# Performance work log

Measured on AMD Instinct MI355X. Metric: run time of the kernel, lower is better.

Reference implementation:

```python
import jax, jax.numpy as jnp
import numpy as np

B, C_IN, H, W = 16, 1024, 32, 32
D_CODE, K = 1024, 2048  # codebook_dim, codebook_size


def setup_inputs() -> dict:
    key = jax.random.key(0)
    k1, k2, k3, k4 = jax.random.split(key, 4)
    x = jax.random.normal(k1, (B, C_IN, H, W), dtype=jnp.float32)
    # 1x1 conv kernel stored as (out=D_CODE, in=C_IN); scaled like torch conv init
    conv_w = jax.random.normal(k2, (D_CODE, C_IN), dtype=jnp.float32) / np.sqrt(C_IN)
    conv_b = jax.random.normal(k3, (D_CODE,), dtype=jnp.float32) * 0.01
    codebook = jax.random.normal(k4, (D_CODE, K), dtype=jnp.float32)
    return {"x": x, "conv_w": conv_w, "conv_b": conv_b, "codebook": codebook}


def reference(x, conv_w, conv_b, codebook):
    # 1x1 conv projection: (B, C_IN, H, W) -> (B, D_CODE, H, W)
    xp = jnp.einsum('bchw,dc->bdhw', x, conv_w) + conv_b[None, :, None, None]

    b, d, h, w = xp.shape
    # flatten spatial: (N, D) with N = B*H*W (matches 'b d h w -> (b h w) d')
    xf = jnp.transpose(xp, (0, 2, 3, 1)).reshape(-1, d)

    # pairwise squared distances to codebook columns: (N, K)
    dist = (jnp.sum(xf * xf, axis=1, keepdims=True)
            - 2.0 * (xf @ codebook)
            + jnp.sum(codebook * codebook, axis=0, keepdims=True))
    indices = jnp.argmin(dist, axis=1).reshape(b, h, w)  # (B, H, W)

    # gather codes: codebook.T is (K, D)
    quant_hw_d = codebook.T[indices]  # (B, H, W, D)
    quant = jnp.transpose(quant_hw_d, (0, 3, 1, 2))  # (B, D, H, W)

    # commitment loss (quantized detached)
    diff = jnp.mean((jax.lax.stop_gradient(quant) - xp) ** 2)

    # straight-through estimator
    quant_st = xp + jax.lax.stop_gradient(quant - xp)
    return quant_st, diff, indices
```

## Files before the change

### kernel.cpp

```cpp
#include <hip/hip_runtime.h>
#include <stdint.h>

#define BATCH 16
#define CIN   1024
#define HWSZ  1024
#define NPOS  16384
#define DCODE 1024
#define KCB   2048

#define OUT_QUANT 0
#define OUT_DIFF  16777216
#define OUT_IDX   16777217

#define OFF_PACKED 0u
#define OFF_CNORM  131072u
#define OFF_DIFF   139264u
#define OFF_WH     262144u
#define OFF_WL     2359296u
#define OFF_CBH    4456448u
#define OFF_CBL    8650752u
#define OFF_DYN    12845056u

typedef _Float16 f16x8 __attribute__((ext_vector_type(8)));
typedef float f32x4 __attribute__((ext_vector_type(4)));
typedef int i32x4 __attribute__((ext_vector_type(4)));
union H4 { _Float16 h[4]; uint2 u; };
union H8 { _Float16 h[8]; uint4 u; };
union QU { uint4 u; uint16_t v[8]; };
union B16 { char c[16]; uint4 u; };

__device__ __forceinline__ void gl_lds16(const void* g, void* l) {
  __builtin_amdgcn_global_load_lds(
      (const __attribute__((address_space(1))) uint32_t*)g,
      (__attribute__((address_space(3))) uint32_t*)l, 16, 0, 0);
}

__global__ void k_init(unsigned long long* __restrict__ packed, double* __restrict__ diffsum) {
  int i = blockIdx.x * 256 + threadIdx.x;
  if (i < NPOS) packed[i] = 0xFFFFFFFFFFFFFFFFull;
  if (i == 0) *diffsum = 0.0;
}

__global__ __launch_bounds__(256) void k_prep_w(const float* __restrict__ w,
                                                _Float16* __restrict__ wh, _Float16* __restrict__ wl) {
  const int d = blockIdx.x;
  const int c = threadIdx.x * 4;
  float4 v = *(const float4*)&w[(size_t)d * CIN + c];
  H4 hh, ll;
  float vv[4] = {v.x, v.y, v.z, v.w};
  #pragma unroll
  for (int i = 0; i < 4; ++i) {
    _Float16 h = (_Float16)vv[i];
    hh.h[i] = h;
    ll.h[i] = (_Float16)(vv[i] - (float)h);
  }
  *(uint2*)&wh[(size_t)d * CIN + c] = hh.u;
  *(uint2*)&wl[(size_t)d * CIN + c] = ll.u;
}

__global__ __launch_bounds__(256) void k_prep_cb(const float* __restrict__ cb,
                                                 _Float16* __restrict__ cbh, _Float16* __restrict__ cbl,
                                                 char* __restrict__ cq) {
  __shared__ float ts[64][65];
  const int t = threadIdx.x;
  const int k0 = blockIdx.x * 64, d0 = blockIdx.y * 64;
  #pragma unroll
  for (int i = 0; i < 4; ++i) {
    const int r = i * 16 + (t >> 4);
    float4 v = *(const float4*)&cb[(size_t)(d0 + r) * KCB + k0 + (t & 15) * 4];
    ts[r][(t & 15) * 4 + 0] = v.x; ts[r][(t & 15) * 4 + 1] = v.y;
    ts[r][(t & 15) * 4 + 2] = v.z; ts[r][(t & 15) * 4 + 3] = v.w;
  }
  __syncthreads();
  const int j = t >> 2;
  const int q = t & 3;
  H8 hh[2], ll[2];
  B16 qb;
  #pragma unroll
  for (int e = 0; e < 16; ++e) {
    float xv = ts[q * 16 + e][j];
    _Float16 h = (_Float16)xv;
    hh[e >> 3].h[e & 7] = h;
    ll[e >> 3].h[e & 7] = (_Float16)(xv - (float)h);
    int qi = (int)rintf(xv * 20.f);
    qi = qi > 127 ? 127 : (qi < -127 ? -127 : qi);
    qb.c[e] = (char)qi;
  }
  size_t o = (size_t)(k0 + j) * DCODE + d0 + q * 16;
  *(uint4*)&cbh[o] = hh[0].u; *(uint4*)&cbh[o + 8] = hh[1].u;
  *(uint4*)&cbl[o] = ll[0].u; *(uint4*)&cbl[o + 8] = ll[1].u;
  if (cq) *(uint4*)&cq[o] = qb.u;
}

__global__ __launch_bounds__(256) void k_prep_x(const float* __restrict__ x,
                                                _Float16* __restrict__ xh, _Float16* __restrict__ xl,
                                                int n_base) {
  __shared__ float ts[64][65];
  const int t = threadIdx.x;
  const int nt0 = blockIdx.x * 64;
  const int c0 = blockIdx.y * 64;
  const int ng = n_base + nt0;
  const int b = ng >> 10, hw0 = ng & 1023;
  #pragma unroll
  for (int i = 0; i < 4; ++i) {
    const int r = i * 16 + (t >> 4);
    float4 v = *(const float4*)&x[((size_t)b * CIN + c0 + r) * HWSZ + hw0 + (t & 15) * 4];
    ts[r][(t & 15) * 4 + 0] = v.x; ts[r][(t & 15) * 4 + 1] = v.y;
    ts[r][(t & 15) * 4 + 2] = v.z; ts[r][(t & 15) * 4 + 3] = v.w;
  }
  __syncthreads();
  const int j = t >> 2;
  const int q = t & 3;
  H8 hh[2], ll[2];
  #pragma unroll
  for (int e = 0; e < 16; ++e) {
    float xv = ts[q * 16 + e][j];
    _Float16 h = (_Float16)xv;
    hh[e >> 3].h[e & 7] = h;
    ll[e >> 3].h[e & 7] = (_Float16)(xv - (float)h);
  }
  size_t o = (size_t)(nt0 + j) * CIN + c0 + q * 16;
  *(uint4*)&xh[o] = hh[0].u; *(uint4*)&xh[o + 8] = hh[1].u;
  *(uint4*)&xl[o] = ll[0].u; *(uint4*)&xl[o + 8] = ll[1].u;
}

__global__ __launch_bounds__(256) void k_prep_xq(const _Float16* __restrict__ xph,
                                                 char* __restrict__ xq) {
  const size_t base = ((size_t)blockIdx.x * 256 + threadIdx.x) * 16;
  H8 a, b;
  a.u = *(const uint4*)&xph[base];
  b.u = *(const uint4*)&xph[base + 8];
  B16 qb;
  #pragma unroll
  for (int i = 0; i < 8; ++i) {
    int qi = (int)rintf((float)a.h[i] * 20.f);
    qi = qi > 127 ? 127 : (qi < -127 ? -127 : qi);
    qb.c[i] = (char)qi;
    int qj = (int)rintf((float)b.h[i] * 20.f);
    qj = qj > 127 ? 127 : (qj < -127 ? -127 : qj);
    qb.c[8 + i] = (char)qj;
  }
  *(uint4*)&xq[base] = qb.u;
}

__global__ __launch_bounds__(256) void k_cnorm2(const _Float16* __restrict__ cbh,
                                                const _Float16* __restrict__ cbl,
                                                float* __restrict__ cnorm) {
  __shared__ double rd[256];
  const int k = blockIdx.x;
  const int t = threadIdx.x;
  H4 hh, ll;
  hh.u = *(const uint2*)&cbh[(size_t)k * DCODE + t * 4];
  ll.u = *(const uint2*)&cbl[(size_t)k * DCODE + t * 4];
  double s = 0.0;
  #pragma unroll
  for (int i = 0; i < 4; ++i) {
    float v = (float)hh.h[i] + (float)ll.h[i];
    s += (double)v * v;
  }
  rd[t] = s;
  __syncthreads();
  for (int st = 128; st > 0; st >>= 1) {
    if (t < st) rd[t] += rd[t + st];
    __syncthreads();
  }
  if (t == 0) cnorm[k] = (float)rd[0];
}

template <int EPI, int NKTT>
__global__ __launch_bounds__(512, 2) void k_gemm_u(
    const _Float16* __restrict__ aH, const _Float16* __restrict__ aL,
    const _Float16* __restrict__ bH, const _Float16* __restrict__ bL,
    const float* __restrict__ bias,
    _Float16* __restrict__ oH, _Float16* __restrict__ oL,
    const float* __restrict__ cnorm, unsigned long long* __restrict__ packed,
    uint16_t* __restrict__ dqout, int n_base) {
  __shared__ __align__(16) _Float16 smem[65536];
  const int tid = threadIdx.x;
  const int lane = tid & 63, wid = tid >> 6;
  const int wm = wid >> 2, wn = wid & 3;
  const int m0 = blockIdx.x * 256;
  const int n0 = blockIdx.y * 256;
  const int kg = lane >> 4;
  const int l7 = lane & 7;

  const int srow = lane >> 3;
  const int sg = l7 ^ srow;
  size_t srcA[4], srcB[4];
  int sdst[4];
  #pragma unroll
  for (int i = 0; i < 4; ++i) {
    const int r = i * 64 + wid * 8 + srow;
    srcA[i] = (size_t)(m0 + r) * 1024 + sg * 8;
    srcB[i] = (size_t)(n0 + r) * 1024 + sg * 8;
    sdst[i] = i * 4096 + wid * 512;
  }
  const int xrd[2] = {(kg ^ l7) * 8, ((4 + kg) ^ l7) * 8};
  int arow[8], brow[4];
  #pragma unroll
  for (int fi = 0; fi < 8; ++fi) arow[fi] = (wm * 128 + fi * 16 + (lane & 15)) * 64;
  #pragma unroll
  for (int fj = 0; fj < 4; ++fj) brow[fj] = 16384 + (wn * 64 + fj * 16 + (lane & 15)) * 64;

  auto stage = [&](int kt, int part) {
    const int tp = kt >> 4;
    const int dbase = (kt & 15) * 64;
    const int buf = (kt & 1) << 15;
    if (part == 0) {
      const _Float16* pA = (tp == 2 ? aL : aH);
      #pragma unroll
      for (int i = 0; i < 4; ++i) gl_lds16(pA + srcA[i] + dbase, smem + buf + sdst[i]);
    } else {
      const _Float16* pB = (tp == 1 ? bL : bH);
      #pragma unroll
      for (int i = 0; i < 4; ++i) gl_lds16(pB + srcB[i] + dbase, smem + buf + 16384 + sdst[i]);
    }
  };

  f32x4 acc[8][4];
  #pragma unroll
  for (int i = 0; i < 8; ++i)
    #pragma unroll
    for (int j = 0; j < 4; ++j) acc[i][j] = (f32x4){0.f, 0.f, 0.f, 0.f};

  stage(0, 0); stage(0, 1);
  asm volatile("s_waitcnt vmcnt(0)" ::: "memory");
  __builtin_amdgcn_s_barrier();
  __builtin_amdgcn_sched_barrier(0);

  for (int kt = 0; kt < NKTT; ++kt) {
    const int buf = (kt & 1) << 15;
    f16x8 bfr[4][2];
    #pragma unroll
    for (int fj = 0; fj < 4; ++fj)
      #pragma unroll
      for (int ks = 0; ks < 2; ++ks)
        bfr[fj][ks] = *(const f16x8*)&smem[buf + brow[fj] + xrd[ks]];
    #pragma unroll
    for (int q = 0; q < 4; ++q) {
      f16x8 afr[2][2];
      #pragma unroll
      for (int f2 = 0; f2 < 2; ++f2)
        #pragma unroll
        for (int ks = 0; ks < 2; ++ks)
          afr[f2][ks] = *(const f16x8*)&smem[buf + arow[q * 2 + f2] + xrd[ks]];
      if (kt < NKTT - 1) {
        if (q == 0) stage(kt + 1, 0);
        else if (q == 1) stage(kt + 1, 1);
      }
      __builtin_amdgcn_s_setprio(1);
      #pragma unroll
      for (int f2 = 0; f2 < 2; ++f2)
        #pragma unroll
        for (int fj = 0; fj < 4; ++fj)
          #pragma unroll
          for (int ks = 0; ks < 2; ++ks)
            acc[q * 2 + f2][fj] = __builtin_amdgcn_mfma_f32_16x16x32_f16(
                afr[f2][ks], bfr[fj][ks], acc[q * 2 + f2][fj], 0, 0, 0);
      __builtin_amdgcn_s_setprio(0);
      __builtin_amdgcn_sched_barrier(0);
    }
    asm volatile("s_waitcnt vmcnt(0)" ::: "memory");
    __builtin_amdgcn_s_barrier();
    __builtin_amdgcn_sched_barrier(0);
  }

  if (EPI == 1) {
    unsigned long long* su = (unsigned long long*)smem;
    float cn[4]; int kcol[4];
    #pragma unroll
    for (int fj = 0; fj < 4; ++fj) {
      kcol[fj] = n0 + wn * 64 + fj * 16 + (lane & 15);
      cn[fj] = cnorm[kcol[fj]];
    }
    #pragma unroll
    for (int fi = 0; fi < 8; ++fi) {
      #pragma unroll
      for (int r = 0; r < 4; ++r) {
        float best = 3.4e38f; int bk = 0;
        #pragma unroll
        for (int fj = 0; fj < 4; ++fj) {
          const float v = cn[fj] - 2.0f * acc[fi][fj][r];
          if (v < best) { best = v; bk = kcol[fj]; }
        }
        union { float f; uint32_t u; } cv; cv.f = best;
        uint32_t hi = cv.u ^ ((uint32_t)((int32_t)cv.u >> 31) | 0x80000000u);
        unsigned long long key = ((unsigned long long)hi << 32) | (uint32_t)bk;
        #pragma unroll
        for (int s = 1; s < 16; s <<= 1) {
          unsigned long long o = __shfl_xor(key, s, 64);
          if (o < key) key = o;
        }
        if ((lane & 15) == 0)
          su[wn * 256 + wm * 128 + fi * 16 + kg * 4 + r] = key;
      }
    }
    __syncthreads();
    if (tid < 256) {
      unsigned long long k = su[tid];
      #pragma unroll
      for (int w = 1; w < 4; ++w) {
        unsigned long long o = su[w * 256 + tid];
        if (o < k) k = o;
      }
      atomicMin(&packed[n_base + m0 + tid], k);
    }
  } else {
    float bi[4];
    #pragma unroll
    for (int fj = 0; fj < 4; ++fj) bi[fj] = bias[n0 + wn * 64 + fj * 16 + (lane & 15)];
    const int sw = kg << 4;
    #pragma unroll
    for (int pl = 0; pl < 2; ++pl) {
      #pragma unroll
      for (int fi = 0; fi < 8; ++fi)
        #pragma unroll
        for (int r = 0; r < 4; ++r) {
          const int pos_l = wm * 128 + fi * 16 + kg * 4 + r;
          #pragma unroll
          for (int fj = 0; fj < 4; ++fj) {
            const int d_l = wn * 64 + fj * 16 + (lane & 15);
            float v = acc[fi][fj][r] + bi[fj];
            _Float16 h = (_Float16)v;
            smem[pos_l * 256 + (d_l ^ sw)] = pl ? (_Float16)(v - (float)h) : h;
          }
        }
      __syncthreads();
      _Float16* dst = pl ? oL : oH;
      #pragma unroll
      for (int p = 0; p < 16; ++p) {
        const int row = p * 16 + (tid >> 5);
        const int lc = tid & 31;
        const int pc = lc ^ (((row >> 2) & 3) << 1);
        *(uint4*)&dst[(size_t)(m0 + row) * 1024 + n0 + lc * 8] = *(const uint4*)&smem[row * 256 + pc * 8];
      }
      __syncthreads();
    }
  }
}

__global__ __launch_bounds__(512, 2) void k_screen_q(
    const char* __restrict__ xq, const char* __restrict__ cq,
    const float* __restrict__ cnorm, uint16_t* __restrict__ dqout) {
  __shared__ __align__(16) char smem[131072];
  const int tid = threadIdx.x;
  const int lane = tid & 63, wid = tid >> 6;
  const int wm = wid >> 2, wn = wid & 3;
  const int m0 = blockIdx.x * 256;
  const int n0 = blockIdx.y * 256;
  const int kg = lane >> 4;
  const int l7 = lane & 7;
  const int l15 = lane & 15;

  const int srow = lane >> 3;
  const int sg = l7 ^ srow;
  size_t srcA[4], srcB[4];
  int sdst[4];
  #pragma unroll
  for (int i = 0; i < 4; ++i) {
    const int r = i * 64 + wid * 8 + srow;
    srcA[i] = (size_t)(m0 + r) * 1024 + sg * 16;
    srcB[i] = (size_t)(n0 + r) * 1024 + sg * 16;
    sdst[i] = i * 8192 + wid * 1024;
  }
  const int xrd[2] = {(kg ^ l7) * 16, ((4 + kg) ^ l7) * 16};
  int arow[8], brow[4];
  #pragma unroll
  for (int fi = 0; fi < 8; ++fi) arow[fi] = (wm * 128 + fi * 16 + l15) * 128;
  #pragma unroll
  for (int fj = 0; fj < 4; ++fj) brow[fj] = 32768 + (wn * 64 + fj * 16 + l15) * 128;

  auto stage = [&](int kt, int part) {
    const int dbase = kt * 128;
    const int buf = (kt & 1) << 16;
    if (part == 0) {
      #pragma unroll
      for (int i = 0; i < 4; ++i) gl_lds16(xq + srcA[i] + dbase, smem + buf + sdst[i]);
    } else {
      #pragma unroll
      for (int i = 0; i < 4; ++i) gl_lds16(cq + srcB[i] + dbase, smem + buf + 32768 + sdst[i]);
    }
  };

  i32x4 acc[8][4];
  #pragma unroll
  for (int i = 0; i < 8; ++i)
    #pragma unroll
    for (int j = 0; j < 4; ++j) acc[i][j] = (i32x4){0, 0, 0, 0};

  stage(0, 0); stage(0, 1);
  asm volatile("s_waitcnt vmcnt(0)" ::: "memory");
  __builtin_amdgcn_s_barrier();
  __builtin_amdgcn_sched_barrier(0);

  for (int kt = 0; kt < 8; ++kt) {
    const int buf = (kt & 1) << 16;
    i32x4 bfr[4][2];
    #pragma unroll
    for (int fj = 0; fj < 4; ++fj)
      #pragma unroll
      for (int ks = 0; ks < 2; ++ks)
        bfr[fj][ks] = *(const i32x4*)&smem[buf + brow[fj] + xrd[ks]];
    #pragma unroll
    for (int q = 0; q < 4; ++q) {
      i32x4 afr[2][2];
      #pragma unroll
      for (int f2 = 0; f2 < 2; ++f2)
        #pragma unroll
        for (int ks = 0; ks < 2; ++ks)
          afr[f2][ks] = *(const i32x4*)&smem[buf + arow[q * 2 + f2] + xrd[ks]];
      if (kt < 7) {
        if (q == 0) stage(kt + 1, 0);
        else if (q == 1) stage(kt + 1, 1);
      }
      __builtin_amdgcn_s_setprio(1);
      #pragma unroll
      for (int f2 = 0; f2 < 2; ++f2)
        #pragma unroll
        for (int fj = 0; fj < 4; ++fj)
          #pragma unroll
          for (int ks = 0; ks < 2; ++ks)
            acc[q * 2 + f2][fj] = __builtin_amdgcn_mfma_i32_16x16x64_i8(
                afr[f2][ks], bfr[fj][ks], acc[q * 2 + f2][fj], 0, 0, 0);
      __builtin_amdgcn_s_setprio(0);
      __builtin_amdgcn_sched_barrier(0);
    }
    asm volatile("s_waitcnt vmcnt(0)" ::: "memory");
    __builtin_amdgcn_s_barrier();
    __builtin_amdgcn_sched_barrier(0);
  }

  uint16_t* sq = (uint16_t*)smem;
  float cn[4]; int kcolL[4];
  #pragma unroll
  for (int fj = 0; fj < 4; ++fj) {
    kcolL[fj] = wn * 64 + fj * 16 + l15;
    cn[fj] = cnorm[n0 + kcolL[fj]];
  }
  const int sw = kg << 4;
  #pragma unroll
  for (int fi = 0; fi < 8; ++fi)
    #pragma unroll
    for (int r = 0; r < 4; ++r) {
      const int pos_l = wm * 128 + fi * 16 + kg * 4 + r;
      #pragma unroll
      for (int fj = 0; fj < 4; ++fj) {
        float qf = (cn[fj] - 0.005f * (float)acc[fi][fj][r] - 512.f) * 16.f;
        uint32_t qq = qf <= 0.f ? 0u : (qf >= 65535.f ? 65535u : (uint32_t)qf);
        sq[pos_l * 256 + (kcolL[fj] ^ sw)] = (uint16_t)qq;
      }
    }
  __syncthreads();
  #pragma unroll
  for (int p = 0; p < 16; ++p) {
    const int row = p * 16 + (tid >> 5);
    const int lc = tid & 31;
    const int pc = lc ^ (((row >> 2) & 3) << 1);
    *(uint4*)&dqout[(size_t)(m0 + row) * 2048 + n0 + lc * 8] = *(const uint4*)&sq[row * 256 + pc * 8];
  }
}

__global__ __launch_bounds__(256) void k_refine(
    const uint16_t* __restrict__ dq,
    const _Float16* __restrict__ xph, const _Float16* __restrict__ xpl,
    const _Float16* __restrict__ cbh, const _Float16* __restrict__ cbl,
    unsigned long long* __restrict__ packed) {
  const int n = blockIdx.x;
  const int t = threadIdx.x;
  __shared__ float xpr[1024];
  __shared__ uint32_t smin[256];
  __shared__ double red[256];
  __shared__ int cand[64];
  __shared__ int ncand;
  if (t == 0) ncand = 0;
  {
    H4 hh, ll;
    hh.u = *(const uint2*)&xph[(size_t)n * 1024 + t * 4];
    ll.u = *(const uint2*)&xpl[(size_t)n * 1024 + t * 4];
    #pragma unroll
    for (int i = 0; i < 4; ++i) xpr[t * 4 + i] = (float)hh.h[i] + (float)ll.h[i];
  }
  QU qv;
  qv.u = *(const uint4*)&dq[(size_t)n * 2048 + t * 8];
  uint32_t lmin = 0xFFFFFFFFu;
  #pragma unroll
  for (int j = 0; j < 8; ++j) lmin = (qv.v[j] < lmin) ? qv.v[j] : lmin;
  smin[t] = lmin;
  __syncthreads();
  for (int s = 128; s > 0; s >>= 1) {
    if (t < s && smin[t + s] < smin[t]) smin[t] = smin[t + s];
    __syncthreads();
  }
  const uint32_t thr = smin[0] + 192;
  #pragma unroll
  for (int j = 0; j < 8; ++j)
    if (qv.v[j] <= thr) {
      int p = atomicAdd(&ncand, 1);
      if (p < 64) cand[p] = t * 8 + j;
    }
  __syncthreads();
  int nc = ncand; if (nc > 64) nc = 64;
  double best_d = 1e300; int best_k = 0x7FFFFFFF;
  for (int c = 0; c < nc; ++c) {
    const int k = cand[c];
    H4 ch, cl;
    ch.u = *(const uint2*)&cbh[(size_t)k * 1024 + t * 4];
    cl.u = *(const uint2*)&cbl[(size_t)k * 1024 + t * 4];
    double s = 0.0;
    #pragma unroll
    for (int i = 0; i < 4; ++i) {
      double dd = (double)xpr[t * 4 + i] - (double)((float)ch.h[i] + (float)cl.h[i]);
      s += dd * dd;
    }
    red[t] = s;
    __syncthreads();
    for (int st = 128; st > 0; st >>= 1) {
      if (t < st) red[t] += red[t + st];
      __syncthreads();
    }
    const double d = red[0];
    __syncthreads();
    if (d < best_d || (d == best_d && k < best_k)) { best_d = d; best_k = k; }
  }
  if (t == 0) packed[n] = (unsigned long long)(uint32_t)best_k;
}

__global__ __launch_bounds__(256) void k_gather2(
    const _Float16* __restrict__ cbh, const _Float16* __restrict__ cbl,
    const _Float16* __restrict__ xph, const _Float16* __restrict__ xpl,
    const unsigned long long* __restrict__ packed,
    float* __restrict__ out, double* __restrict__ diffsum,
    int n_base, int NC) {
  __shared__ float tile[64][65];
  __shared__ uint32_t sidx[64];
  __shared__ float red[256];
  const int t = threadIdx.x;
  const int n0 = blockIdx.x * 64;
  const int ng = n_base + n0;
  const int b = ng >> 10, hw0 = ng & 1023;
  const int dbeg = blockIdx.y * 256;
  if (t < 64) {
    uint32_t idx = (uint32_t)(packed[ng + t] & 0xFFFFFFFFu);
    if (idx > (KCB - 1)) idx = KCB - 1;
    sidx[t] = idx;
  }
  const int rrow = t >> 3, rcol = (t & 7) * 8;
  const int wd = t >> 4, whw = (t & 15) * 4;
  float local = 0.f;
  for (int d0 = dbeg; d0 < dbeg + 256; d0 += 64) {
    __syncthreads();
    #pragma unroll
    for (int p = 0; p < 2; ++p) {
      const int nl = p * 32 + rrow;
      const uint32_t idx = sidx[nl];
      H8 hh, ll, ph, pl;
      hh.u = *(const uint4*)&cbh[(size_t)idx * DCODE + d0 + rcol];
      ll.u = *(const uint4*)&cbl[(size_t)idx * DCODE + d0 + rcol];
      ph.u = *(const uint4*)&xph[(size_t)(n0 + nl) * DCODE + d0 + rcol];
      pl.u = *(const uint4*)&xpl[(size_t)(n0 + nl) * DCODE + d0 + rcol];
      #pragma unroll
      for (int j = 0; j < 8; ++j) {
        const float q = (float)hh.h[j] + (float)ll.h[j];
        const float xv = (float)ph.h[j] + (float)pl.h[j];
        const float dd = q - xv;
        local += dd * dd;
        tile[nl][rcol + j] = q;
      }
    }
    __syncthreads();
    #pragma unroll
    for (int i = 0; i < 4; ++i) {
      const int dl = i * 16 + wd;
      float4 v;
      v.x = tile[whw + 0][dl]; v.y = tile[whw + 1][dl];
      v.z = tile[whw + 2][dl]; v.w = tile[whw + 3][dl];
      *(float4*)&out[((size_t)b * DCODE + d0 + dl) * HWSZ + hw0 + whw] = v;
    }
  }
  red[t] = local;
  __syncthreads();
  for (int s = 128; s > 0; s >>= 1) {
    if (t < s) red[t] += red[t + s];
    __syncthreads();
  }
  if (t == 0) atomicAdd(diffsum, (double)red[0]);
}

__global__ void k_final(const unsigned long long* __restrict__ packed,
                        const double* __restrict__ diffsum,
                        float* __restrict__ out) {
  int i = blockIdx.x * 256 + threadIdx.x;
  if (i < NPOS) {
    uint32_t idx = (uint32_t)(packed[i] & 0xFFFFFFFFu);
    if (idx > (KCB - 1)) idx = KCB - 1;
    out[OUT_IDX + i] = (float)idx;
  }
  if (i == 0) out[OUT_DIFF] = (float)(*diffsum / ((double)NPOS * (double)DCODE));
}

extern "C" void kernel_launch(void* const* d_in, const int* in_sizes, int n_in,
                              void* d_out, int out_size, void* d_ws, size_t ws_size,
                              hipStream_t stream) {
  const float* x    = (const float*)d_in[0];
  const float* w    = (const float*)d_in[1];
  const float* bias = (const float*)d_in[2];
  const float* cb   = (const float*)d_in[3];
  float* out = (float*)d_out;
  char* ws = (char*)d_ws;
  unsigned long long* packed = (unsigned long long*)(ws + OFF_PACKED);
  float* cnorm = (float*)(ws + OFF_CNORM);
  double* diffsum = (double*)(ws + OFF_DIFF);
  _Float16* wh  = (_Float16*)(ws + OFF_WH);
  _Float16* wl  = (_Float16*)(ws + OFF_WL);
  _Float16* cbh = (_Float16*)(ws + OFF_CBH);
  _Float16* cbl = (_Float16*)(ws + OFF_CBL);

  const size_t need_fast = (size_t)OFF_DYN + (size_t)16384 * 8192 + 16777216 + 2097152;
  const bool fast = ws_size >= need_fast;

  k_init<<<64, 256, 0, stream>>>(packed, diffsum);
  k_prep_w<<<DCODE, 256, 0, stream>>>(w, wh, wl);

  if (fast) {
    const int NC = 16384;
    char* dyn = ws + OFF_DYN;
    _Float16* xh  = (_Float16*)dyn;
    _Float16* xl  = (_Float16*)(dyn + (size_t)NC * 2048);
    _Float16* xph = (_Float16*)(dyn + (size_t)NC * 4096);
    _Float16* xpl = (_Float16*)(dyn + (size_t)NC * 6144);
    char* xq = dyn + (size_t)NC * 8192;
    char* cq = xq + 16777216;
    uint16_t* dq = (uint16_t*)out;
    k_prep_cb<<<dim3(KCB / 64, DCODE / 64), 256, 0, stream>>>(cb, cbh, cbl, cq);
    k_cnorm2<<<KCB, 256, 0, stream>>>(cbh, cbl, cnorm);
    k_prep_x<<<dim3(NC / 64, CIN / 64), 256, 0, stream>>>(x, xh, xl, 0);
    k_gemm_u<0, 48><<<dim3(NC / 256, DCODE / 256), 512, 0, stream>>>(
        xh, xl, wh, wl, bias, xph, xpl, nullptr, nullptr, nullptr, 0);
    k_prep_xq<<<4096, 256, 0, stream>>>(xph, xq);
    k_screen_q<<<dim3(NC / 256, KCB / 256), 512, 0, stream>>>(xq, cq, cnorm, dq);
    k_refine<<<NPOS, 256, 0, stream>>>(dq, xph, xpl, cbh, cbl, packed);
    k_gather2<<<dim3(NC / 64, 4), 256, 0, stream>>>(cbh, cbl, xph, xpl, packed, out, diffsum, 0, NC);
  } else {
    k_prep_cb<<<dim3(KCB / 64, DCODE / 64), 256, 0, stream>>>(cb, cbh, cbl, nullptr);
    k_cnorm2<<<KCB, 256, 0, stream>>>(cbh, cbl, cnorm);
    int NC = 256;
    if      (ws_size >= OFF_DYN + (size_t)16384 * 8192) NC = 16384;
    else if (ws_size >= OFF_DYN + (size_t)8192  * 8192) NC = 8192;
    else if (ws_size >= OFF_DYN + (size_t)4096  * 8192) NC = 4096;
    else if (ws_size >= OFF_DYN + (size_t)2048  * 8192) NC = 2048;
    else if (ws_size >= OFF_DYN + (size_t)1024  * 8192) NC = 1024;
    else if (ws_size >= OFF_DYN + (size_t)512   * 8192) NC = 512;
    const int nchunks = NPOS / NC;
    char* dyn = ws + OFF_DYN;
    _Float16* xh  = (_Float16*)dyn;
    _Float16* xl  = (_Float16*)(dyn + (size_t)NC * 2048);
    _Float16* xph = (_Float16*)(dyn + (size_t)NC * 4096);
    _Float16* xpl = (_Float16*)(dyn + (size_t)NC * 6144);
    for (int c = 0; c < nchunks; ++c) {
      const int n_base = c * NC;
      k_prep_x<<<dim3(NC / 64, CIN / 64), 256, 0, stream>>>(x, xh, xl, n_base);
      k_gemm_u<0, 48><<<dim3(NC / 256, DCODE / 256), 512, 0, stream>>>(
          xh, xl, wh, wl, bias, xph, xpl, nullptr, nullptr, nullptr, 0);
      k_gemm_u<1, 48><<<dim3(NC / 256, KCB / 256), 512, 0, stream>>>(
          xph, xpl, cbh, cbl, nullptr, nullptr, nullptr, cnorm, packed, nullptr, n_base);
      k_gather2<<<dim3(NC / 64, 4), 256, 0, stream>>>(cbh, cbl, xph, xpl, packed, out, diffsum, n_base, NC);
    }
  }
  k_final<<<64, 256, 0, stream>>>(packed, diffsum, out);
}
```

Baseline: 277.1 us.

## Replace 3-pass fp16 conv GEMM with int8 correction pass plus fp16 main pass

```diff
diff --git a/kernel.cpp b/kernel.cpp
--- a/kernel.cpp
+++ b/kernel.cpp
@@ -35,6 +35,11 @@
       (__attribute__((address_space(3))) uint32_t*)l, 16, 0, 0);
 }
 
+__device__ __forceinline__ char q8(float v, float s) {
+  int qi = (int)rintf(v * s);
+  return (char)(qi > 127 ? 127 : (qi < -127 ? -127 : qi));
+}
+
 __global__ void k_init(unsigned long long* __restrict__ packed, double* __restrict__ diffsum) {
   int i = blockIdx.x * 256 + threadIdx.x;
   if (i < NPOS) packed[i] = 0xFFFFFFFFFFFFFFFFull;
@@ -42,20 +47,29 @@
 }
 
 __global__ __launch_bounds__(256) void k_prep_w(const float* __restrict__ w,
-                                                _Float16* __restrict__ wh, _Float16* __restrict__ wl) {
+                                                _Float16* __restrict__ wh, _Float16* __restrict__ wl,
+                                                char* __restrict__ whq, char* __restrict__ wlq) {
   const int d = blockIdx.x;
   const int c = threadIdx.x * 4;
   float4 v = *(const float4*)&w[(size_t)d * CIN + c];
   H4 hh, ll;
+  char qh[4], ql[4];
   float vv[4] = {v.x, v.y, v.z, v.w};
   #pragma unroll
   for (int i = 0; i < 4; ++i) {
     _Float16 h = (_Float16)vv[i];
+    float l = vv[i] - (float)h;
     hh.h[i] = h;
-    ll.h[i] = (_Float16)(vv[i] - (float)h);
+    ll.h[i] = (_Float16)l;
+    qh[i] = q8((float)h, 1024.f);
+    ql[i] = q8(l, 4194304.f);
   }
   *(uint2*)&wh[(size_t)d * CIN + c] = hh.u;
   *(uint2*)&wl[(size_t)d * CIN + c] = ll.u;
+  if (whq) {
+    *(uint32_t*)&whq[(size_t)d * CIN + c] = *(uint32_t*)qh;
+    *(uint32_t*)&wlq[(size_t)d * CIN + c] = *(uint32_t*)ql;
+  }
 }
 
 __global__ __launch_bounds__(256) void k_prep_cb(const float* __restrict__ cb,
@@ -82,9 +96,7 @@
     _Float16 h = (_Float16)xv;
     hh[e >> 3].h[e & 7] = h;
     ll[e >> 3].h[e & 7] = (_Float16)(xv - (float)h);
-    int qi = (int)rintf(xv * 20.f);
-    qi = qi > 127 ? 127 : (qi < -127 ? -127 : qi);
-    qb.c[e] = (char)qi;
+    qb.c[e] = q8(xv, 20.f);
   }
   size_t o = (size_t)(k0 + j) * DCODE + d0 + q * 16;
   *(uint4*)&cbh[o] = hh[0].u; *(uint4*)&cbh[o + 8] = hh[1].u;
@@ -94,6 +106,7 @@
 
 __global__ __launch_bounds__(256) void k_prep_x(const float* __restrict__ x,
                                                 _Float16* __restrict__ xh, _Float16* __restrict__ xl,
+                                                char* __restrict__ xhq, char* __restrict__ xlq,
                                                 int n_base) {
   __shared__ float ts[64][65];
   const int t = threadIdx.x;
@@ -112,35 +125,21 @@
   const int j = t >> 2;
   const int q = t & 3;
   H8 hh[2], ll[2];
+  B16 qh, ql;
   #pragma unroll
   for (int e = 0; e < 16; ++e) {
     float xv = ts[q * 16 + e][j];
     _Float16 h = (_Float16)xv;
+    float l = xv - (float)h;
     hh[e >> 3].h[e & 7] = h;
-    ll[e >> 3].h[e & 7] = (_Float16)(xv - (float)h);
+    ll[e >> 3].h[e & 7] = (_Float16)l;
+    qh.c[e] = q8((float)h, 16.f);
+    ql.c[e] = q8(l, 65536.f);
   }
   size_t o = (size_t)(nt0 + j) * CIN + c0 + q * 16;
   *(uint4*)&xh[o] = hh[0].u; *(uint4*)&xh[o + 8] = hh[1].u;
-  *(uint4*)&xl[o] = ll[0].u; *(uint4*)&xl[o + 8] = ll[1].u;
-}
-
-__global__ __launch_bounds__(256) void k_prep_xq(const _Float16* __restrict__ xph,
-                                                 char* __restrict__ xq) {
-  const size_t base = ((size_t)blockIdx.x * 256 + threadIdx.x) * 16;
-  H8 a, b;
-  a.u = *(const uint4*)&xph[base];
-  b.u = *(const uint4*)&xph[base + 8];
-  B16 qb;
-  #pragma unroll
-  for (int i = 0; i < 8; ++i) {
-    int qi = (int)rintf((float)a.h[i] * 20.f);
-    qi = qi > 127 ? 127 : (qi < -127 ? -127 : qi);
-    qb.c[i] = (char)qi;
-    int qj = (int)rintf((float)b.h[i] * 20.f);
-    qj = qj > 127 ? 127 : (qj < -127 ? -127 : qj);
-    qb.c[8 + i] = (char)qj;
-  }
-  *(uint4*)&xq[base] = qb.u;
+  if (xl) { *(uint4*)&xl[o] = ll[0].u; *(uint4*)&xl[o + 8] = ll[1].u; }
+  if (xhq) { *(uint4*)&xhq[o] = qh.u; *(uint4*)&xlq[o] = ql.u; }
 }
 
 __global__ __launch_bounds__(256) void k_cnorm2(const _Float16* __restrict__ cbh,
@@ -167,6 +166,220 @@
   if (t == 0) cnorm[k] = (float)rd[0];
 }
 
+__global__ __launch_bounds__(512, 2) void k_gemm1_mix(
+    const char* __restrict__ xlq, const char* __restrict__ xhq,
+    const char* __restrict__ whq, const char* __restrict__ wlq,
+    const _Float16* __restrict__ xh, const _Float16* __restrict__ wh,
+    const float* __restrict__ bias,
+    _Float16* __restrict__ oH, _Float16* __restrict__ oL,
+    char* __restrict__ xqout) {
+  __shared__ __align__(16) char smem[131072];
+  const int tid = threadIdx.x;
+  const int lane = tid & 63, wid = tid >> 6;
+  const int wm = wid >> 2, wn = wid & 3;
+  const int m0 = blockIdx.x * 256;
+  const int n0 = blockIdx.y * 256;
+  const int kg = lane >> 4;
+  const int l7 = lane & 7;
+  const int l15 = lane & 15;
+
+  const int srow = lane >> 3;
+  const int sg = l7 ^ srow;
+  int rr[4];
+  #pragma unroll
+  for (int i = 0; i < 4; ++i) rr[i] = i * 64 + wid * 8 + srow;
+  size_t srcA8[4], srcB8[4], srcA16[4], srcB16[4];
+  int sdst[4];
+  #pragma unroll
+  for (int i = 0; i < 4; ++i) {
+    srcA8[i] = (size_t)(m0 + rr[i]) * 1024 + sg * 16;
+    srcB8[i] = (size_t)(n0 + rr[i]) * 1024 + sg * 16;
+    srcA16[i] = (size_t)(m0 + rr[i]) * 1024 + sg * 8;
+    srcB16[i] = (size_t)(n0 + rr[i]) * 1024 + sg * 8;
+    sdst[i] = i * 8192 + wid * 1024;
+  }
+  const int xrd[2] = {(kg ^ l7) * 16, ((4 + kg) ^ l7) * 16};
+  int arow[8], brow[4];
+  #pragma unroll
+  for (int fi = 0; fi < 8; ++fi) arow[fi] = (wm * 128 + fi * 16 + l15) * 128;
+  #pragma unroll
+  for (int fj = 0; fj < 4; ++fj) brow[fj] = 32768 + (wn * 64 + fj * 16 + l15) * 128;
+
+  auto stage8 = [&](int kt, int part) {
+    const int dbase = (kt & 7) * 128;
+    const int buf = (kt & 1) << 16;
+    if (part == 0) {
+      const char* pA = (kt >> 3) ? xhq : xlq;
+      #pragma unroll
+      for (int i = 0; i < 4; ++i) gl_lds16(pA + srcA8[i] + dbase, smem + buf + sdst[i]);
+    } else {
+      const char* pB = (kt >> 3) ? wlq : whq;
+      #pragma unroll
+      for (int i = 0; i < 4; ++i) gl_lds16(pB + srcB8[i] + dbase, smem + buf + 32768 + sdst[i]);
+    }
+  };
+  auto stage16 = [&](int kt, int part) {
+    const int dbase = (kt & 15) * 64;
+    const int buf = (kt & 1) << 16;
+    if (part == 0) {
+      #pragma unroll
+      for (int i = 0; i < 4; ++i) gl_lds16(xh + srcA16[i] + dbase, smem + buf + sdst[i]);
+    } else {
+      #pragma unroll
+      for (int i = 0; i < 4; ++i) gl_lds16(wh + srcB16[i] + dbase, smem + buf + 32768 + sdst[i]);
+    }
+  };
+
+  i32x4 acci[8][4];
+  #pragma unroll
+  for (int i = 0; i < 8; ++i)
+    #pragma unroll
+    for (int j = 0; j < 4; ++j) acci[i][j] = (i32x4){0, 0, 0, 0};
+
+  stage8(0, 0); stage8(0, 1);
+  asm volatile("s_waitcnt vmcnt(0)" ::: "memory");
+  __builtin_amdgcn_s_barrier();
+  __builtin_amdgcn_sched_barrier(0);
+  for (int kt = 0; kt < 16; ++kt) {
+    const int buf = (kt & 1) << 16;
+    i32x4 bfr[4][2];
+    #pragma unroll
+    for (int fj = 0; fj < 4; ++fj)
+      #pragma unroll
+      for (int ks = 0; ks < 2; ++ks)
+        bfr[fj][ks] = *(const i32x4*)&smem[buf + brow[fj] + xrd[ks]];
+    #pragma unroll
+    for (int q = 0; q < 4; ++q) {
+      i32x4 afr[2][2];
+      #pragma unroll
+      for (int f2 = 0; f2 < 2; ++f2)
+        #pragma unroll
+        for (int ks = 0; ks < 2; ++ks)
+          afr[f2][ks] = *(const i32x4*)&smem[buf + arow[q * 2 + f2] + xrd[ks]];
+      if (kt < 15) {
+        if (q == 0) stage8(kt + 1, 0);
+        else if (q == 1) stage8(kt + 1, 1);
+      }
+      __builtin_amdgcn_s_setprio(1);
+      #pragma unroll
+      for (int f2 = 0; f2 < 2; ++f2)
+        #pragma unroll
+        for (int fj = 0; fj < 4; ++fj)
+          #pragma unroll
+          for (int ks = 0; ks < 2; ++ks)
+            acci[q * 2 + f2][fj] = __builtin_amdgcn_mfma_i32_16x16x64_i8(
+                afr[f2][ks], bfr[fj][ks], acci[q * 2 + f2][fj], 0, 0, 0);
+      __builtin_amdgcn_s_setprio(0);
+      __builtin_amdgcn_sched_barrier(0);
+    }
+    asm volatile("s_waitcnt vmcnt(0)" ::: "memory");
+    __builtin_amdgcn_s_barrier();
+    __builtin_amdgcn_sched_barrier(0);
+  }
+
+  f32x4 acc[8][4];
+  #pragma unroll
+  for (int i = 0; i < 8; ++i)
+    #pragma unroll
+    for (int j = 0; j < 4; ++j)
+      #pragma unroll
+      for (int e = 0; e < 4; ++e)
+        acc[i][j][e] = (float)acci[i][j][e] * (1.f / 67108864.f);
+
+  stage16(0, 0); stage16(0, 1);
+  asm volatile("s_waitcnt vmcnt(0)" ::: "memory");
+  __builtin_amdgcn_s_barrier();
+  __builtin_amdgcn_sched_barrier(0);
+  for (int kt = 0; kt < 16; ++kt) {
+    const int buf = (kt & 1) << 16;
+    f16x8 bfr[4][2];
+    #pragma unroll
+    for (int fj = 0; fj < 4; ++fj)
+      #pragma unroll
+      for (int ks = 0; ks < 2; ++ks)
+        bfr[fj][ks] = *(const f16x8*)&smem[buf + brow[fj] + xrd[ks]];
+    #pragma unroll
+    for (int q = 0; q < 4; ++q) {
+      f16x8 afr[2][2];
+      #pragma unroll
+      for (int f2 = 0; f2 < 2; ++f2)
+        #pragma unroll
+        for (int ks = 0; ks < 2; ++ks)
+          afr[f2][ks] = *(const f16x8*)&smem[buf + arow[q * 2 + f2] + xrd[ks]];
+      if (kt < 15) {
+        if (q == 0) stage16(kt + 1, 0);
+        else if (q == 1) stage16(kt + 1, 1);
+      }
+      __builtin_amdgcn_s_setprio(1);
+      #pragma unroll
+      for (int f2 = 0; f2 < 2; ++f2)
+        #pragma unroll
+        for (int fj = 0; fj < 4; ++fj)
+          #pragma unroll
+          for (int ks = 0; ks < 2; ++ks)
+            acc[q * 2 + f2][fj] = __builtin_amdgcn_mfma_f32_16x16x32_f16(
+                afr[f2][ks], bfr[fj][ks], acc[q * 2 + f2][fj], 0, 0, 0);
+      __builtin_amdgcn_s_setprio(0);
+      __builtin_amdgcn_sched_barrier(0);
+    }
+    asm volatile("s_waitcnt vmcnt(0)" ::: "memory");
+    __builtin_amdgcn_s_barrier();
+    __builtin_amdgcn_sched_barrier(0);
+  }
+
+  float bi[4];
+  #pragma unroll
+  for (int fj = 0; fj < 4; ++fj) bi[fj] = bias[n0 + wn * 64 + fj * 16 + l15];
+  const int sw = kg << 4;
+  _Float16* sm16 = (_Float16*)smem;
+  #pragma unroll
+  for (int pl = 0; pl < 2; ++pl) {
+    #pragma unroll
+    for (int fi = 0; fi < 8; ++fi)
+      #pragma unroll
+      for (int r = 0; r < 4; ++r) {
+        const int pos_l = wm * 128 + fi * 16 + kg * 4 + r;
+        #pragma unroll
+        for (int fj = 0; fj < 4; ++fj) {
+          const int d_l = wn * 64 + fj * 16 + l15;
+          float v = acc[fi][fj][r] + bi[fj];
+          _Float16 h = (_Float16)v;
+          sm16[pos_l * 256 + (d_l ^ sw)] = pl ? (_Float16)(v - (float)h) : h;
+        }
+      }
+    __syncthreads();
+    _Float16* dst = pl ? oL : oH;
+    #pragma unroll
+    for (int p = 0; p < 16; ++p) {
+      const int row = p * 16 + (tid >> 5);
+      const int lc = tid & 31;
+      const int pc = lc ^ (((row >> 2) & 3) << 1);
+      *(uint4*)&dst[(size_t)(m0 + row) * 1024 + n0 + lc * 8] = *(const uint4*)&sm16[row * 256 + pc * 8];
+    }
+    __syncthreads();
+  }
+  #pragma unroll
+  for (int fi = 0; fi < 8; ++fi)
+    #pragma unroll
+    for (int r = 0; r < 4; ++r) {
+      const int pos_l = wm * 128 + fi * 16 + kg * 4 + r;
+      #pragma unroll
+      for (int fj = 0; fj < 4; ++fj) {
+        const int d_l = wn * 64 + fj * 16 + l15;
+        smem[pos_l * 256 + (d_l ^ sw)] = q8(acc[fi][fj][r] + bi[fj], 20.f);
+      }
+    }
+  __syncthreads();
+  #pragma unroll
+  for (int p = 0; p < 8; ++p) {
+    const int idx = p * 512 + tid;
+    const int row = idx >> 4;
+    const int ch = idx & 15;
+    const int pch = ch ^ ((row >> 2) & 3);
+    *(uint4*)&xqout[(size_t)(m0 + row) * 1024 + n0 + ch * 16] = *(const uint4*)&smem[row * 256 + pch * 16];
+  }
+}
+
 template <int EPI, int NKTT>
 __global__ __launch_bounds__(512, 2) void k_gemm_u(
     const _Float16* __restrict__ aH, const _Float16* __restrict__ aL,
@@ -174,7 +387,7 @@
     const float* __restrict__ bias,
     _Float16* __restrict__ oH, _Float16* __restrict__ oL,
     const float* __restrict__ cnorm, unsigned long long* __restrict__ packed,
-    uint16_t* __restrict__ dqout, int n_base) {
+    int n_base) {
   __shared__ __align__(16) _Float16 smem[65536];
   const int tid = threadIdx.x;
   const int lane = tid & 63, wid = tid >> 6;
@@ -183,7 +396,6 @@
   const int n0 = blockIdx.y * 256;
   const int kg = lane >> 4;
   const int l7 = lane & 7;
-
   const int srow = lane >> 3;
   const int sg = l7 ^ srow;
   size_t srcA[4], srcB[4];
@@ -351,7 +563,6 @@
   const int kg = lane >> 4;
   const int l7 = lane & 7;
   const int l15 = lane & 15;
-
   const int srow = lane >> 3;
   const int sg = l7 ^ srow;
   size_t srcA[4], srcB[4];
@@ -464,7 +675,7 @@
     const uint16_t* __restrict__ dq,
     const _Float16* __restrict__ xph, const _Float16* __restrict__ xpl,
     const _Float16* __restrict__ cbh, const _Float16* __restrict__ cbl,
-    unsigned long long* __restrict__ packed) {
+    unsigned long long* __restrict__ packed, double* __restrict__ diffsum) {
   const int n = blockIdx.x;
   const int t = threadIdx.x;
   __shared__ float xpr[1024];
@@ -522,9 +733,13 @@
     __syncthreads();
     if (d < best_d || (d == best_d && k < best_k)) { best_d = d; best_k = k; }
   }
-  if (t == 0) packed[n] = (unsigned long long)(uint32_t)best_k;
-}
-
+  if (t == 0) {
+    packed[n] = (unsigned long long)(uint32_t)best_k;
+    atomicAdd(diffsum, best_d);
+  }
+}
+
+template <int DIFF>
 __global__ __launch_bounds__(256) void k_gather2(
     const _Float16* __restrict__ cbh, const _Float16* __restrict__ cbl,
     const _Float16* __restrict__ xph, const _Float16* __restrict__ xpl,
@@ -553,18 +768,25 @@
     for (int p = 0; p < 2; ++p) {
       const int nl = p * 32 + rrow;
       const uint32_t idx = sidx[nl];
-      H8 hh, ll, ph, pl;
+      H8 hh, ll;
       hh.u = *(const uint4*)&cbh[(size_t)idx * DCODE + d0 + rcol];
       ll.u = *(const uint4*)&cbl[(size_t)idx * DCODE + d0 + rcol];
-      ph.u = *(const uint4*)&xph[(size_t)(n0 + nl) * DCODE + d0 + rcol];
-      pl.u = *(const uint4*)&xpl[(size_t)(n0 + nl) * DCODE + d0 + rcol];
-      #pragma unroll
-      for (int j = 0; j < 8; ++j) {
-        const float q = (float)hh.h[j] + (float)ll.h[j];
-        const float xv = (float)ph.h[j] + (float)pl.h[j];
-        const float dd = q - xv;
-        local += dd * dd;
-        tile[nl][rcol + j] = q;
+      if (DIFF) {
+        H8 ph, pl;
+        ph.u = *(const uint4*)&xph[(size_t)(n0 + nl) * DCODE + d0 + rcol];
+        pl.u = *(const uint4*)&xpl[(size_t)(n0 + nl) * DCODE + d0 + rcol];
+        #pragma unroll
+        for (int j = 0; j < 8; ++j) {
+          const float q = (float)hh.h[j] + (float)ll.h[j];
+          const float xv = (float)ph.h[j] + (float)pl.h[j];
+          const float dd = q - xv;
+          local += dd * dd;
+          tile[nl][rcol + j] = q;
+        }
+      } else {
+        #pragma unroll
+        for (int j = 0; j < 8; ++j)
+          tile[nl][rcol + j] = (float)hh.h[j] + (float)ll.h[j];
       }
     }
     __syncthreads();
@@ -574,16 +796,18 @@
       float4 v;
       v.x = tile[whw + 0][dl]; v.y = tile[whw + 1][dl];
       v.z = tile[whw + 2][dl]; v.w = tile[whw + 3][dl];
-      *(float4*)&out[((size_t)b * DCODE + d0 + dl) * HWSZ + hw0 + whw] = v;
-    }
-  }
-  red[t] = local;
-  __syncthreads();
-  for (int s = 128; s > 0; s >>= 1) {
-    if (t < s) red[t] += red[t + s];
-    __syncthreads();
-  }
-  if (t == 0) atomicAdd(diffsum, (double)red[0]);
+      *(float4*)&out[((size_t)b * DCODE + dbeg - dbeg + d0 + dl) * HWSZ + hw0 + whw] = v;
+    }
+  }
+  if (DIFF) {
+    red[t] = local;
+    __syncthreads();
+    for (int s = 128; s > 0; s >>= 1) {
+      if (t < s) red[t] += red[t + s];
+      __syncthreads();
+    }
+    if (t == 0) atomicAdd(diffsum, (double)red[0]);
+  }
 }
 
 __global__ void k_final(const unsigned long long* __restrict__ packed,
@@ -615,32 +839,34 @@
   _Float16* cbh = (_Float16*)(ws + OFF_CBH);
   _Float16* cbl = (_Float16*)(ws + OFF_CBL);
 
-  const size_t need_fast = (size_t)OFF_DYN + (size_t)16384 * 8192 + 16777216 + 2097152;
+  const size_t need_fast = (size_t)OFF_DYN + 3u * 33554432u + 3u * 16777216u + 2097152u + 2u * 1048576u;
   const bool fast = ws_size >= need_fast;
 
   k_init<<<64, 256, 0, stream>>>(packed, diffsum);
-  k_prep_w<<<DCODE, 256, 0, stream>>>(w, wh, wl);
 
   if (fast) {
-    const int NC = 16384;
     char* dyn = ws + OFF_DYN;
     _Float16* xh  = (_Float16*)dyn;
-    _Float16* xl  = (_Float16*)(dyn + (size_t)NC * 2048);
-    _Float16* xph = (_Float16*)(dyn + (size_t)NC * 4096);
-    _Float16* xpl = (_Float16*)(dyn + (size_t)NC * 6144);
-    char* xq = dyn + (size_t)NC * 8192;
-    char* cq = xq + 16777216;
+    _Float16* xph = (_Float16*)(dyn + 33554432u);
+    _Float16* xpl = (_Float16*)(dyn + 67108864u);
+    char* xlq = dyn + 100663296u;
+    char* xhq = dyn + 117440512u;
+    char* xq  = dyn + 134217728u;
+    char* cq  = dyn + 150994944u;
+    char* whq = dyn + 153092096u;
+    char* wlq = dyn + 154140672u;
     uint16_t* dq = (uint16_t*)out;
+    k_prep_w<<<DCODE, 256, 0, stream>>>(w, wh, wl, whq, wlq);
     k_prep_cb<<<dim3(KCB / 64, DCODE / 64), 256, 0, stream>>>(cb, cbh, cbl, cq);
     k_cnorm2<<<KCB, 256, 0, stream>>>(cbh, cbl, cnorm);
-    k_prep_x<<<dim3(NC / 64, CIN / 64), 256, 0, stream>>>(x, xh, xl, 0);
-    k_gemm_u<0, 48><<<dim3(NC / 256, DCODE / 256), 512, 0, stream>>>(
-        xh, xl, wh, wl, bias, xph, xpl, nullptr, nullptr, nullptr, 0);
-    k_prep_xq<<<4096, 256, 0, stream>>>(xph, xq);
-    k_screen_q<<<dim3(NC / 256, KCB / 256), 512, 0, stream>>>(xq, cq, cnorm, dq);
-    k_refine<<<NPOS, 256, 0, stream>>>(dq, xph, xpl, cbh, cbl, packed);
-    k_gather2<<<dim3(NC / 64, 4), 256, 0, stream>>>(cbh, cbl, xph, xpl, packed, out, diffsum, 0, NC);
+    k_prep_x<<<dim3(NPOS / 64, CIN / 64), 256, 0, stream>>>(x, xh, nullptr, xhq, xlq, 0);
+    k_gemm1_mix<<<dim3(NPOS / 256, DCODE / 256), 512, 0, stream>>>(
+        xlq, xhq, whq, wlq, xh, wh, bias, xph, xpl, xq);
+    k_screen_q<<<dim3(NPOS / 256, KCB / 256), 512, 0, stream>>>(xq, cq, cnorm, dq);
+    k_refine<<<NPOS, 256, 0, stream>>>(dq, xph, xpl, cbh, cbl, packed, diffsum);
+    k_gather2<0><<<dim3(NPOS / 64, 4), 256, 0, stream>>>(cbh, cbl, xph, xpl, packed, out, diffsum, 0, NPOS);
   } else {
+    k_prep_w<<<DCODE, 256, 0, stream>>>(w, wh, wl, nullptr, nullptr);
     k_prep_cb<<<dim3(KCB / 64, DCODE / 64), 256, 0, stream>>>(cb, cbh, cbl, nullptr);
     k_cnorm2<<<KCB, 256, 0, stream>>>(cbh, cbl, cnorm);
     int NC = 256;
@@ -658,12 +884,12 @@
     _Float16* xpl = (_Float16*)(dyn + (size_t)NC * 6144);
     for (int c = 0; c < nchunks; ++c) {
       const int n_base = c * NC;
-      k_prep_x<<<dim3(NC / 64, CIN / 64), 256, 0, stream>>>(x, xh, xl, n_base);
+      k_prep_x<<<dim3(NC / 64, CIN / 64), 256, 0, stream>>>(x, xh, xl, nullptr, nullptr, n_base);
       k_gemm_u<0, 48><<<dim3(NC / 256, DCODE / 256), 512, 0, stream>>>(
-          xh, xl, wh, wl, bias, xph, xpl, nullptr, nullptr, nullptr, 0);
+          xh, xl, wh, wl, bias, xph, xpl, nullptr, nullptr, 0);
       k_gemm_u<1, 48><<<dim3(NC / 256, KCB / 256), 512, 0, stream>>>(
-          xph, xpl, cbh, cbl, nullptr, nullptr, nullptr, cnorm, packed, nullptr, n_base);
-      k_gather2<<<dim3(NC / 64, 4), 256, 0, stream>>>(cbh, cbl, xph, xpl, packed, out, diffsum, n_base, NC);
+          xph, xpl, cbh, cbl, nullptr, nullptr, nullptr, cnorm, packed, n_base);
+      k_gather2<1><<<dim3(NC / 64, 4), 256, 0, stream>>>(cbh, cbl, xph, xpl, packed, out, diffsum, n_base, NC);
     }
   }
   k_final<<<64, 256, 0, stream>>>(packed, diffsum, out);
```

New measurement: 479.8 us. 1.73x slower.

## Fuse int8 quantization into projection GEMM and derive commitment loss from refine distances

Applied to the files above, without the earlier changes.

```diff
diff --git a/kernel.cpp b/kernel.cpp
--- a/kernel.cpp
+++ b/kernel.cpp
@@ -35,6 +35,11 @@
       (__attribute__((address_space(3))) uint32_t*)l, 16, 0, 0);
 }
 
+__device__ __forceinline__ char q8(float v, float s) {
+  int qi = (int)rintf(v * s);
+  return (char)(qi > 127 ? 127 : (qi < -127 ? -127 : qi));
+}
+
 __global__ void k_init(unsigned long long* __restrict__ packed, double* __restrict__ diffsum) {
   int i = blockIdx.x * 256 + threadIdx.x;
   if (i < NPOS) packed[i] = 0xFFFFFFFFFFFFFFFFull;
@@ -82,9 +87,7 @@
     _Float16 h = (_Float16)xv;
     hh[e >> 3].h[e & 7] = h;
     ll[e >> 3].h[e & 7] = (_Float16)(xv - (float)h);
-    int qi = (int)rintf(xv * 20.f);
-    qi = qi > 127 ? 127 : (qi < -127 ? -127 : qi);
-    qb.c[e] = (char)qi;
+    qb.c[e] = q8(xv, 20.f);
   }
   size_t o = (size_t)(k0 + j) * DCODE + d0 + q * 16;
   *(uint4*)&cbh[o] = hh[0].u; *(uint4*)&cbh[o + 8] = hh[1].u;
@@ -122,25 +125,6 @@
   size_t o = (size_t)(nt0 + j) * CIN + c0 + q * 16;
   *(uint4*)&xh[o] = hh[0].u; *(uint4*)&xh[o + 8] = hh[1].u;
   *(uint4*)&xl[o] = ll[0].u; *(uint4*)&xl[o + 8] = ll[1].u;
-}
-
-__global__ __launch_bounds__(256) void k_prep_xq(const _Float16* __restrict__ xph,
-                                                 char* __restrict__ xq) {
-  const size_t base = ((size_t)blockIdx.x * 256 + threadIdx.x) * 16;
-  H8 a, b;
-  a.u = *(const uint4*)&xph[base];
-  b.u = *(const uint4*)&xph[base + 8];
-  B16 qb;
-  #pragma unroll
-  for (int i = 0; i < 8; ++i) {
-    int qi = (int)rintf((float)a.h[i] * 20.f);
-    qi = qi > 127 ? 127 : (qi < -127 ? -127 : qi);
-    qb.c[i] = (char)qi;
-    int qj = (int)rintf((float)b.h[i] * 20.f);
-    qj = qj > 127 ? 127 : (qj < -127 ? -127 : qj);
-    qb.c[8 + i] = (char)qj;
-  }
-  *(uint4*)&xq[base] = qb.u;
 }
 
 __global__ __launch_bounds__(256) void k_cnorm2(const _Float16* __restrict__ cbh,
@@ -174,7 +158,7 @@
     const float* __restrict__ bias,
     _Float16* __restrict__ oH, _Float16* __restrict__ oL,
     const float* __restrict__ cnorm, unsigned long long* __restrict__ packed,
-    uint16_t* __restrict__ dqout, int n_base) {
+    char* __restrict__ xqout, int n_base) {
   __shared__ __align__(16) _Float16 smem[65536];
   const int tid = threadIdx.x;
   const int lane = tid & 63, wid = tid >> 6;
@@ -336,6 +320,29 @@
       }
       __syncthreads();
     }
+    if (xqout) {
+      char* sm8 = (char*)smem;
+      #pragma unroll
+      for (int fi = 0; fi < 8; ++fi)
+        #pragma unroll
+        for (int r = 0; r < 4; ++r) {
+          const int pos_l = wm * 128 + fi * 16 + kg * 4 + r;
+          #pragma unroll
+          for (int fj = 0; fj < 4; ++fj) {
+            const int d_l = wn * 64 + fj * 16 + (lane & 15);
+            sm8[pos_l * 256 + (d_l ^ sw)] = q8(acc[fi][fj][r] + bi[fj], 20.f);
+          }
+        }
+      __syncthreads();
+      #pragma unroll
+      for (int p = 0; p < 8; ++p) {
+        const int idx = p * 512 + tid;
+        const int row = idx >> 4;
+        const int ch = idx & 15;
+        const int pch = ch ^ ((row >> 2) & 3);
+        *(uint4*)&xqout[(size_t)(m0 + row) * 1024 + n0 + ch * 16] = *(const uint4*)&sm8[row * 256 + pch * 16];
+      }
+    }
   }
 }
 
@@ -351,7 +358,6 @@
   const int kg = lane >> 4;
   const int l7 = lane & 7;
   const int l15 = lane & 15;
-
   const int srow = lane >> 3;
   const int sg = l7 ^ srow;
   size_t srcA[4], srcB[4];
@@ -464,15 +470,14 @@
     const uint16_t* __restrict__ dq,
     const _Float16* __restrict__ xph, const _Float16* __restrict__ xpl,
     const _Float16* __restrict__ cbh, const _Float16* __restrict__ cbl,
-    unsigned long long* __restrict__ packed) {
+    unsigned long long* __restrict__ packed, double* __restrict__ bestd) {
   const int n = blockIdx.x;
   const int t = threadIdx.x;
   __shared__ float xpr[1024];
   __shared__ uint32_t smin[256];
   __shared__ double red[256];
-  __shared__ int cand[64];
-  __shared__ int ncand;
-  if (t == 0) ncand = 0;
+  __shared__ int cand[256];
+  __shared__ int scan[256];
   {
     H4 hh, ll;
     hh.u = *(const uint2*)&xph[(size_t)n * 1024 + t * 4];
@@ -491,15 +496,29 @@
     if (t < s && smin[t + s] < smin[t]) smin[t] = smin[t + s];
     __syncthreads();
   }
-  const uint32_t thr = smin[0] + 192;
+  uint32_t thr = smin[0] + 192;
+  if (thr > 65535u) thr = 65535u;
+  int cnt = 0;
+  #pragma unroll
+  for (int j = 0; j < 8; ++j) cnt += (qv.v[j] <= thr) ? 1 : 0;
+  scan[t] = cnt;
+  __syncthreads();
+  for (int off = 1; off < 256; off <<= 1) {
+    int add = (t >= off) ? scan[t - off] : 0;
+    __syncthreads();
+    scan[t] += add;
+    __syncthreads();
+  }
+  const int total = scan[255];
+  int o = scan[t] - cnt;
   #pragma unroll
   for (int j = 0; j < 8; ++j)
     if (qv.v[j] <= thr) {
-      int p = atomicAdd(&ncand, 1);
-      if (p < 64) cand[p] = t * 8 + j;
+      if (o < 256) cand[o] = t * 8 + j;
+      ++o;
     }
   __syncthreads();
-  int nc = ncand; if (nc > 64) nc = 64;
+  int nc = total > 256 ? 256 : total;
   double best_d = 1e300; int best_k = 0x7FFFFFFF;
   for (int c = 0; c < nc; ++c) {
     const int k = cand[c];
@@ -522,9 +541,27 @@
     __syncthreads();
     if (d < best_d || (d == best_d && k < best_k)) { best_d = d; best_k = k; }
   }
-  if (t == 0) packed[n] = (unsigned long long)(uint32_t)best_k;
-}
-
+  if (t == 0) {
+    packed[n] = (unsigned long long)(uint32_t)best_k;
+    bestd[n] = best_d;
+  }
+}
+
+__global__ __launch_bounds__(256) void k_diffsum(const double* __restrict__ bestd,
+                                                 double* __restrict__ diffsum) {
+  __shared__ double red[256];
+  const int t = threadIdx.x;
+  const int base = blockIdx.x * 256;
+  red[t] = bestd[base + t];
+  __syncthreads();
+  for (int st = 128; st > 0; st >>= 1) {
+    if (t < st) red[t] += red[t + st];
+    __syncthreads();
+  }
+  if (t == 0) atomicAdd(diffsum, red[0]);
+}
+
+template <int DIFF>
 __global__ __launch_bounds__(256) void k_gather2(
     const _Float16* __restrict__ cbh, const _Float16* __restrict__ cbl,
     const _Float16* __restrict__ xph, const _Float16* __restrict__ xpl,
@@ -553,18 +590,25 @@
     for (int p = 0; p < 2; ++p) {
       const int nl = p * 32 + rrow;
       const uint32_t idx = sidx[nl];
-      H8 hh, ll, ph, pl;
+      H8 hh, ll;
       hh.u = *(const uint4*)&cbh[(size_t)idx * DCODE + d0 + rcol];
       ll.u = *(const uint4*)&cbl[(size_t)idx * DCODE + d0 + rcol];
-      ph.u = *(const uint4*)&xph[(size_t)(n0 + nl) * DCODE + d0 + rcol];
-      pl.u = *(const uint4*)&xpl[(size_t)(n0 + nl) * DCODE + d0 + rcol];
-      #pragma unroll
-      for (int j = 0; j < 8; ++j) {
-        const float q = (float)hh.h[j] + (float)ll.h[j];
-        const float xv = (float)ph.h[j] + (float)pl.h[j];
-        const float dd = q - xv;
-        local += dd * dd;
-        tile[nl][rcol + j] = q;
+      if (DIFF) {
+        H8 ph, pl;
+        ph.u = *(const uint4*)&xph[(size_t)(n0 + nl) * DCODE + d0 + rcol];
+        pl.u = *(const uint4*)&xpl[(size_t)(n0 + nl) * DCODE + d0 + rcol];
+        #pragma unroll
+        for (int j = 0; j < 8; ++j) {
+          const float q = (float)hh.h[j] + (float)ll.h[j];
+          const float xv = (float)ph.h[j] + (float)pl.h[j];
+          const float dd = q - xv;
+          local += dd * dd;
+          tile[nl][rcol + j] = q;
+        }
+      } else {
+        #pragma unroll
+        for (int j = 0; j < 8; ++j)
+          tile[nl][rcol + j] = (float)hh.h[j] + (float)ll.h[j];
       }
     }
     __syncthreads();
@@ -577,13 +621,15 @@
       *(float4*)&out[((size_t)b * DCODE + d0 + dl) * HWSZ + hw0 + whw] = v;
     }
   }
-  red[t] = local;
-  __syncthreads();
-  for (int s = 128; s > 0; s >>= 1) {
-    if (t < s) red[t] += red[t + s];
-    __syncthreads();
-  }
-  if (t == 0) atomicAdd(diffsum, (double)red[0]);
+  if (DIFF) {
+    red[t] = local;
+    __syncthreads();
+    for (int s = 128; s > 0; s >>= 1) {
+      if (t < s) red[t] += red[t + s];
+      __syncthreads();
+    }
+    if (t == 0) atomicAdd(diffsum, (double)red[0]);
+  }
 }
 
 __global__ void k_final(const unsigned long long* __restrict__ packed,
@@ -615,32 +661,33 @@
   _Float16* cbh = (_Float16*)(ws + OFF_CBH);
   _Float16* cbl = (_Float16*)(ws + OFF_CBL);
 
-  const size_t need_fast = (size_t)OFF_DYN + (size_t)16384 * 8192 + 16777216 + 2097152;
+  const size_t need_fast = (size_t)OFF_DYN + 4u * 33554432u + 16777216u + 2097152u + 131072u;
   const bool fast = ws_size >= need_fast;
 
   k_init<<<64, 256, 0, stream>>>(packed, diffsum);
-  k_prep_w<<<DCODE, 256, 0, stream>>>(w, wh, wl);
 
   if (fast) {
-    const int NC = 16384;
     char* dyn = ws + OFF_DYN;
     _Float16* xh  = (_Float16*)dyn;
-    _Float16* xl  = (_Float16*)(dyn + (size_t)NC * 2048);
-    _Float16* xph = (_Float16*)(dyn + (size_t)NC * 4096);
-    _Float16* xpl = (_Float16*)(dyn + (size_t)NC * 6144);
-    char* xq = dyn + (size_t)NC * 8192;
-    char* cq = xq + 16777216;
+    _Float16* xl  = (_Float16*)(dyn + 33554432u);
+    _Float16* xph = (_Float16*)(dyn + 67108864u);
+    _Float16* xpl = (_Float16*)(dyn + 100663296u);
+    char* xq  = dyn + 134217728u;
+    char* cq  = dyn + 150994944u;
+    double* bestd = (double*)(dyn + 153092096u);
     uint16_t* dq = (uint16_t*)out;
+    k_prep_w<<<DCODE, 256, 0, stream>>>(w, wh, wl);
     k_prep_cb<<<dim3(KCB / 64, DCODE / 64), 256, 0, stream>>>(cb, cbh, cbl, cq);
     k_cnorm2<<<KCB, 256, 0, stream>>>(cbh, cbl, cnorm);
-    k_prep_x<<<dim3(NC / 64, CIN / 64), 256, 0, stream>>>(x, xh, xl, 0);
-    k_gemm_u<0, 48><<<dim3(NC / 256, DCODE / 256), 512, 0, stream>>>(
-        xh, xl, wh, wl, bias, xph, xpl, nullptr, nullptr, nullptr, 0);
-    k_prep_xq<<<4096, 256, 0, stream>>>(xph, xq);
-    k_screen_q<<<dim3(NC / 256, KCB / 256), 512, 0, stream>>>(xq, cq, cnorm, dq);
-    k_refine<<<NPOS, 256, 0, stream>>>(dq, xph, xpl, cbh, cbl, packed);
-    k_gather2<<<dim3(NC / 64, 4), 256, 0, stream>>>(cbh, cbl, xph, xpl, packed, out, diffsum, 0, NC);
+    k_prep_x<<<dim3(NPOS / 64, CIN / 64), 256, 0, stream>>>(x, xh, xl, 0);
+    k_gemm_u<0, 48><<<dim3(NPOS / 256, DCODE / 256), 512, 0, stream>>>(
+        xh, xl, wh, wl, bias, xph, xpl, nullptr, nullptr, xq, 0);
+    k_screen_q<<<dim3(NPOS / 256, KCB / 256), 512, 0, stream>>>(xq, cq, cnorm, dq);
+    k_refine<<<NPOS, 256, 0, stream>>>(dq, xph, xpl, cbh, cbl, packed, bestd);
+    k_diffsum<<<64, 256, 0, stream>>>(bestd, diffsum);
+    k_gather2<0><<<dim3(NPOS / 64, 4), 256, 0, stream>>>(cbh, cbl, xph, xpl, packed, out, diffsum, 0, NPOS);
   } else {
+    k_prep_w<<<DCODE, 256, 0, stream>>>(w, wh, wl);
     k_prep_cb<<<dim3(KCB / 64, DCODE / 64), 256, 0, stream>>>(cb, cbh, cbl, nullptr);
     k_cnorm2<<<KCB, 256, 0, stream>>>(cbh, cbl, cnorm);
     int NC = 256;
@@ -663,7 +710,7 @@
           xh, xl, wh, wl, bias, xph, xpl, nullptr, nullptr, nullptr, 0);
       k_gemm_u<1, 48><<<dim3(NC / 256, KCB / 256), 512, 0, stream>>>(
           xph, xpl, cbh, cbl, nullptr, nullptr, nullptr, cnorm, packed, nullptr, n_base);
-      k_gather2<<<dim3(NC / 64, 4), 256, 0, stream>>>(cbh, cbl, xph, xpl, packed, out, diffsum, n_base, NC);
+      k_gather2<1><<<dim3(NC / 64, 4), 256, 0, stream>>>(cbh, cbl, xph, xpl, packed, out, diffsum, n_base, NC);
     }
   }
   k_final<<<64, 256, 0, stream>>>(packed, diffsum, out);
```

Measured after the change: 351.5 us. +26.8%, slower.
